# Kernel optimization log

Hardware: AMD Instinct MI355X
Metric: run time of the kernel (lower is better)

## Reference

```python
import jax, jax.numpy as jnp
import numpy as np

N = 50000
E = 800000
IN_CH = 256
ADIM = 64
EDIM = 16
NUM_CLUSTERS = 8


def setup_inputs() -> dict:
    key = jax.random.key(0)
    ks = jax.random.split(key, 16)
    def lin(k, fan_in, fan_out):
        w = jax.random.normal(k, (fan_in, fan_out), jnp.float32) * (fan_in ** -0.5)
        b = jnp.zeros((fan_out,), jnp.float32)
        return w, b
    W_down, b_down = lin(ks[0], IN_CH, ADIM)
    W_up, b_up = lin(ks[1], ADIM, IN_CH)
    W_time, b_time = lin(ks[2], EDIM, ADIM)
    Wq, bq = lin(ks[3], ADIM, ADIM)
    Wk, bk = lin(ks[4], ADIM, ADIM)
    Wv, bv = lin(ks[5], ADIM, ADIM)
    W_out, b_out = lin(ks[6], ADIM, ADIM)
    cluster_emb = jax.random.normal(ks[7], (NUM_CLUSTERS, ADIM), jnp.float32)
    x = jax.random.normal(ks[8], (N, IN_CH), jnp.float32)
    edge_attr = jax.random.normal(ks[9], (E, EDIM), jnp.float32)
    edge_index = jax.random.randint(ks[10], (2, E), 0, N, jnp.int32)
    return {"x": x, "edge_attr": edge_attr, "edge_index": edge_index,
            "W_down": W_down, "b_down": b_down, "W_up": W_up, "b_up": b_up,
            "W_time": W_time, "b_time": b_time, "Wq": Wq, "bq": bq,
            "Wk": Wk, "bk": bk, "Wv": Wv, "bv": bv,
            "cluster_emb": cluster_emb, "W_out": W_out, "b_out": b_out}


def reference(x, edge_attr, edge_index, W_down, b_down, W_up, b_up,
              W_time, b_time, Wq, bq, Wk, bk, Wv, bv, cluster_emb, W_out, b_out):
    n_nodes = x.shape[0]
    scaling = ADIM ** -0.5

    node_feat = jax.nn.relu(x @ W_down + b_down)              # [N, D]
    time_feat = jax.nn.relu(edge_attr @ W_time + b_time)      # [E, D]

    q = node_feat @ Wq + bq                                   # [N, D]
    k = time_feat @ Wk + bk                                   # [E, D]
    v = time_feat @ Wv + bv                                   # [E, D]

    # cluster assignment: argmax of softmax(sim) == argmax of sim
    sims = (time_feat @ cluster_emb.T) * scaling              # [E, C]
    cluster = jnp.argmax(sims, axis=-1).astype(jnp.int32)     # [E]

    src = edge_index[0]                                       # [E]
    q_i = q[src]                                              # [E, D]
    attn = jnp.sum(q_i * k, axis=-1) * scaling                # [E]

    # per-(cluster, src) segments replicate the per-cluster loop exactly
    seg = cluster * n_nodes + src                             # [E]
    num_seg = NUM_CLUSTERS * n_nodes

    # scatter_softmax within each (cluster, src) group (numerically stable)
    m = jax.ops.segment_max(attn, seg, num_segments=num_seg)
    ex = jnp.exp(attn - m[seg])
    denom = jax.ops.segment_sum(ex, seg, num_segments=num_seg)
    w = ex / denom[seg]                                       # [E]

    wv = v * w[:, None]                                       # [E, D]
    sums = jax.ops.segment_sum(wv, seg, num_segments=num_seg)
    sums = sums.reshape(NUM_CLUSTERS, n_nodes, ADIM)
    counts = jax.ops.segment_sum(jnp.ones((E,), jnp.float32), seg, num_segments=num_seg)
    counts = counts.reshape(NUM_CLUSTERS, n_nodes)
    mean = sums / jnp.maximum(counts, 1.0)[..., None]         # scatter_mean (0 where empty)

    # divide by number of non-empty clusters (len(outputs) in torch loop)
    edges_per_cluster = jax.ops.segment_sum(jnp.ones((E,), jnp.float32), cluster,
                                            num_segments=NUM_CLUSTERS)
    n_nonempty = jnp.sum((edges_per_cluster > 0).astype(jnp.float32))
    combined = jnp.sum(mean, axis=0) / n_nonempty             # [N, D]

    fused = jax.nn.relu(combined @ W_out + b_out)             # [N, D]
    out = x + (fused @ W_up + b_up)                           # [N, in_ch]
    return out
```

## Files before the change

kernel.cpp:

```cpp
#include <hip/hip_runtime.h>

#define NN 50000
#define EE 800000
#define INCH 256
#define D 64
#define ED 16
#define NC 8
#define NB 196
#define NEGINF (-3.0e38f)

__device__ __align__(16) char g_ws[64u << 20];

typedef __attribute__((ext_vector_type(8))) short bf16x8;
typedef __attribute__((ext_vector_type(4))) float f32x4;

__device__ __forceinline__ unsigned short f2b(float f){
  unsigned u = __float_as_uint(f);
  return (unsigned short)((u + 0x7fffu + ((u >> 16) & 1u)) >> 16);
}
__device__ __forceinline__ unsigned packbf(float lo, float hi){
  return (unsigned)f2b(lo) | ((unsigned)f2b(hi) << 16);
}
__device__ __forceinline__ float blo(unsigned w){ return __uint_as_float(w << 16); }
__device__ __forceinline__ float bhi(unsigned w){ return __uint_as_float(w & 0xffff0000u); }

union FragU { unsigned u[4]; uint4 q; bf16x8 b; };
__device__ __forceinline__ bf16x8 as_frag(unsigned a, unsigned b, unsigned c, unsigned d){
  FragU t; t.u[0]=a; t.u[1]=b; t.u[2]=c; t.u[3]=d; return t.b;
}
__device__ __forceinline__ bf16x8 ld_frag(const unsigned* p){
  FragU t; t.q = *(const uint4*)p; return t.b;
}
__device__ __forceinline__ void split2(float a, float b, unsigned &hi, unsigned &lo){
  hi = packbf(a, b);
  lo = packbf(a - blo(hi), b - bhi(hi));
}
__device__ __forceinline__ void mk_frags(float4 e0, float4 e1, bf16x8 &Ah, bf16x8 &Al){
  unsigned h0,h1,h2,h3,l0,l1,l2,l3;
  split2(e0.x, e0.y, h0, l0);
  split2(e0.z, e0.w, h1, l1);
  split2(e1.x, e1.y, h2, l2);
  split2(e1.z, e1.w, h3, l3);
  Ah = as_frag(h0,h1,h2,h3);
  Al = as_frag(l0,l1,l2,l3);
}

__global__ __launch_bounds__(256) void Adapter_30872224923942_kernel(
    unsigned* __restrict__ ws, int nwords)
{
  int stride = gridDim.x * 256;
  for (int i = blockIdx.x * 256 + threadIdx.x; i < nwords; i += stride)
    ws[i] = 0u;
}

__global__ __launch_bounds__(256) void kpre(
    const float* __restrict__ Wq, const float* __restrict__ bq,
    const float* __restrict__ Wk, const float* __restrict__ bk,
    const float* __restrict__ Wv, const float* __restrict__ bv,
    const float* __restrict__ Wo, const float* __restrict__ Wd,
    const float* __restrict__ Wu,
    float* __restrict__ cvec, float* __restrict__ u,
    float* __restrict__ s0, float* __restrict__ Wvo, float* __restrict__ bvo,
    unsigned* __restrict__ WdTP, unsigned* __restrict__ WuP,
    unsigned* __restrict__ MThP, unsigned* __restrict__ MTlP)
{
  int b = blockIdx.x, t = threadIdx.x;
  if (b < 16){
    int i = b*4 + (t >> 6), j = t & 63;
    float acc = 0.0f;
    for (int d = 0; d < D; ++d) acc = fmaf(Wv[i*D+d], Wo[d*D+j], acc);
    Wvo[i*D+j] = acc;
  } else if (b < 20){
    for (int k = 0; k < 8; ++k){
      int idx = (b-16)*2048 + t*8 + k;
      int col = idx >> 7, kw = idx & 127;
      WdTP[idx] = packbf(Wd[(2*kw)*D + col], Wd[(2*kw+1)*D + col]);
    }
  } else if (b < 24){
    for (int k = 0; k < 8; ++k){
      int idx = (b-20)*2048 + t*8 + k;
      int d2 = idx >> 8, c = idx & 255;
      WuP[idx] = packbf(Wu[(2*d2)*INCH + c], Wu[(2*d2+1)*INCH + c]);
    }
  } else if (b < 26){
    for (int k = 0; k < 4; ++k){
      int idx = (b-24)*1024 + t*4 + k;
      int j = idx >> 5, kw = idx & 31;
      float m0 = 0.0f, m1 = 0.0f;
      for (int d = 0; d < D; ++d) m0 = fmaf(Wq[(2*kw  )*D+d], Wk[j*D+d], m0);
      for (int d = 0; d < D; ++d) m1 = fmaf(Wq[(2*kw+1)*D+d], Wk[j*D+d], m1);
      unsigned hi = packbf(m0, m1);
      MThP[idx] = hi;
      MTlP[idx] = packbf(m0 - blo(hi), m1 - bhi(hi));
    }
  } else {
    if (t < 64){
      float acc = 0.0f;
      for (int d = 0; d < D; ++d) acc = fmaf(Wk[t*D+d], bq[d], acc);
      cvec[t] = acc;
    } else if (t < 128){
      int i = t - 64; float acc = 0.0f;
      for (int d = 0; d < D; ++d) acc = fmaf(Wq[i*D+d], bk[d], acc);
      u[i] = acc;
    } else if (t < 192){
      int j = t - 128; float acc = 0.0f;
      for (int d = 0; d < D; ++d) acc = fmaf(bv[d], Wo[d*D+j], acc);
      bvo[j] = acc;
    } else if (t == 192){
      float acc = 0.0f;
      for (int d = 0; d < D; ++d) acc = fmaf(bq[d], bk[d], acc);
      s0[0] = acc;
    }
  }
}

__global__ __launch_bounds__(256) void p1_hist(
    const int* __restrict__ eidx, int* __restrict__ cnt)
{
  int e = blockIdx.x * 256 + threadIdx.x;
  if (e < EE) atomicAdd(&cnt[eidx[e]], 1);
}

__global__ __launch_bounds__(256) void s1_scan(
    const int* __restrict__ cnt, int* __restrict__ rowptr, int* __restrict__ bsum)
{
  __shared__ int s[256];
  int t = threadIdx.x;
  int i = blockIdx.x * 256 + t;
  int v = (i < NN) ? cnt[i] : 0;
  s[t] = v; __syncthreads();
  #pragma unroll
  for (int off = 1; off < 256; off <<= 1){
    int add = (t >= off) ? s[t - off] : 0;
    __syncthreads();
    s[t] += add;
    __syncthreads();
  }
  if (i < NN) rowptr[i] = s[t] - v;
  if (t == 255) bsum[blockIdx.x] = s[255];
}
__global__ __launch_bounds__(256) void s2_scan(int* __restrict__ bsum)
{
  __shared__ int s[256];
  int t = threadIdx.x;
  int v = (t < NB) ? bsum[t] : 0;
  s[t] = v; __syncthreads();
  #pragma unroll
  for (int off = 1; off < 256; off <<= 1){
    int add = (t >= off) ? s[t - off] : 0;
    __syncthreads();
    s[t] += add;
    __syncthreads();
  }
  if (t < NB) bsum[t] = s[t] - v;
}
__global__ __launch_bounds__(256) void s3_add(
    int* __restrict__ rowptr, const int* __restrict__ bsum)
{
  int i = blockIdx.x * 256 + threadIdx.x;
  if (i < NN) rowptr[i] += bsum[blockIdx.x];
  if (i == 0) rowptr[NN] = EE;
}

__global__ __launch_bounds__(256) void p2_build(
    const int* __restrict__ eidx, const int* __restrict__ rowptr,
    int* __restrict__ fill, int2* __restrict__ pairS)
{
  int e = blockIdx.x * 256 + threadIdx.x;
  if (e >= EE) return;
  int src = eidx[e];
  int r = atomicAdd(&fill[src], 1);
  int2 pr; pr.x = e; pr.y = src;
  pairS[rowptr[src] + r] = pr;
}

__global__ __launch_bounds__(256) void k1_node(
    const float* __restrict__ x, const unsigned* __restrict__ WdTP,
    const float* __restrict__ bd,
    const unsigned* __restrict__ MThP, const unsigned* __restrict__ MTlP,
    const float* __restrict__ cvec, const float* __restrict__ u,
    const float* __restrict__ s0p,
    unsigned short* __restrict__ qkH, float* __restrict__ qb)
{
  __shared__ unsigned sWdT[8192];
  __shared__ unsigned sMTh[2048];
  __shared__ unsigned sMTl[2048];
  __shared__ float sNf[4][16][68];
  int t = threadIdx.x;
  int lane = t & 63;
  int w = t >> 6;
  int colA = lane & 15;
  int g = lane >> 4;
  int row0 = blockIdx.x * 64 + w * 16;

  int arow = row0 + colA;
  const float* xp = x + (size_t)min(arow, NN-1) * INCH + (g << 3);
  float4 xv[16];
  #pragma unroll
  for (int s = 0; s < 8; ++s){
    xv[2*s  ] = ((const float4*)(xp + s*32))[0];
    xv[2*s+1] = ((const float4*)(xp + s*32))[1];
  }
  #pragma unroll
  for (int i = 0; i < 8; ++i){
    int idx = 4*(t + 256*i);
    int col = idx >> 7;
    int dst = (idx & ~127) | ((idx & 127) ^ ((col & 7) << 2));
    *(uint4*)&sWdT[dst] = ((const uint4*)WdTP)[t + 256*i];
  }
  #pragma unroll
  for (int i = 0; i < 2; ++i){
    int idx = 4*(t + 256*i);
    int col = idx >> 5;
    int dst = (idx & ~31) | ((idx & 31) ^ ((col & 7) << 2));
    *(uint4*)&sMTh[dst] = ((const uint4*)MThP)[t + 256*i];
    *(uint4*)&sMTl[dst] = ((const uint4*)MTlP)[t + 256*i];
  }
  __syncthreads();

  f32x4 acc[4];
  #pragma unroll
  for (int nt = 0; nt < 4; ++nt){
    float bdc = bd[nt*16 + colA];
    acc[nt] = (f32x4){bdc, bdc, bdc, bdc};
  }
  #pragma unroll
  for (int s = 0; s < 8; ++s){
    bf16x8 Ah, Al;
    mk_frags(xv[2*s], xv[2*s+1], Ah, Al);
    #pragma unroll
    for (int nt = 0; nt < 4; ++nt){
      int col = nt*16 + colA;
      int kw = s*16 + g*4;
      bf16x8 B = ld_frag(&sWdT[col*128 + (kw ^ ((col & 7) << 2))]);
      acc[nt] = __builtin_amdgcn_mfma_f32_16x16x32_bf16(Ah, B, acc[nt], 0, 0, 0);
      acc[nt] = __builtin_amdgcn_mfma_f32_16x16x32_bf16(Al, B, acc[nt], 0, 0, 0);
    }
  }
  #pragma unroll
  for (int nt = 0; nt < 4; ++nt){
    #pragma unroll
    for (int q = 0; q < 4; ++q)
      sNf[w][g*4 + q][nt*16 + colA] = fmaxf(acc[nt][q], 0.0f);
  }

  {
    const float* nr = &sNf[w][colA][g*16];
    float b = 0.0f;
    #pragma unroll
    for (int c = 0; c < 16; ++c) b = fmaf(nr[c], u[g*16 + c], b);
    b += __shfl_xor(b, 16);
    b += __shfl_xor(b, 32);
    int qrow = row0 + colA;
    if (lane < 16 && qrow < NN) qb[qrow] = b + s0p[0];
  }

  f32x4 acc2[4];
  #pragma unroll
  for (int nt = 0; nt < 4; ++nt){
    float cvl = cvec[nt*16 + colA];
    acc2[nt] = (f32x4){cvl, cvl, cvl, cvl};
  }
  #pragma unroll
  for (int s = 0; s < 2; ++s){
    const float* ar = &sNf[w][colA][s*32 + g*8];
    float4 e0 = *(const float4*)(ar);
    float4 e1 = *(const float4*)(ar + 4);
    bf16x8 Ah, Al;
    mk_frags(e0, e1, Ah, Al);
    #pragma unroll
    for (int nt = 0; nt < 4; ++nt){
      int col = nt*16 + colA;
      int kw = s*16 + g*4;
      bf16x8 Bh = ld_frag(&sMTh[col*32 + (kw ^ ((col & 7) << 2))]);
      bf16x8 Bl = ld_frag(&sMTl[col*32 + (kw ^ ((col & 7) << 2))]);
      acc2[nt] = __builtin_amdgcn_mfma_f32_16x16x32_bf16(Ah, Bh, acc2[nt], 0, 0, 0);
      acc2[nt] = __builtin_amdgcn_mfma_f32_16x16x32_bf16(Al, Bh, acc2[nt], 0, 0, 0);
      acc2[nt] = __builtin_amdgcn_mfma_f32_16x16x32_bf16(Ah, Bl, acc2[nt], 0, 0, 0);
    }
  }
  #pragma unroll
  for (int nt = 0; nt < 4; ++nt){
    #pragma unroll
    for (int q = 0; q < 4; ++q){
      int r = row0 + g*4 + q;
      if (r < NN) qkH[(size_t)r * D + nt*16 + colA] = f2b(acc2[nt][q]);
    }
  }
}

__global__ __launch_bounds__(256) void p3_edge(
    const float* __restrict__ ea, const int* __restrict__ eidx,
    const float* __restrict__ Wt, const float* __restrict__ bt, const float* __restrict__ ce,
    const unsigned short* __restrict__ qkH, const float* __restrict__ qb,
    float* __restrict__ attnE, unsigned char* __restrict__ clE,
    unsigned* __restrict__ epc)
{
  __shared__ unsigned s_epc[NC];
  int t = threadIdx.x;
  if (t < NC) s_epc[t] = 0u;
  __syncthreads();
  int e0 = blockIdx.x * 512 + t;
  int e1 = e0 + 256;
  bool v1 = (e1 < EE);
  int e1c = v1 ? e1 : e0;
  int sA = eidx[e0];
  int sB = eidx[e1c];
  const float4* pa = (const float4*)(ea + (size_t)e0 * ED);
  float4 A0 = pa[0], A1 = pa[1], A2 = pa[2], A3 = pa[3];
  float qb0 = qb[sA];
  const float4* pb = (const float4*)(ea + (size_t)e1c * ED);
  float4 B0 = pb[0], B1 = pb[1], B2 = pb[2], B3 = pb[3];
  float qb1 = qb[sB];
  uint4 QA[8], QB[8];
  {
    const uint4* qp = (const uint4*)(qkH + (size_t)sA * D);
    #pragma unroll
    for (int i = 0; i < 8; ++i) QA[i] = qp[i];
  }
  {
    const uint4* qp = (const uint4*)(qkH + (size_t)sB * D);
    #pragma unroll
    for (int i = 0; i < 8; ++i) QB[i] = qp[i];
  }
  const float4* Wt4 = (const float4*)Wt;
  const float4* bt4 = (const float4*)bt;
  const float4* ce4 = (const float4*)ce;

  {
    float eav[ED] = {A0.x,A0.y,A0.z,A0.w, A1.x,A1.y,A1.z,A1.w,
                     A2.x,A2.y,A2.z,A2.w, A3.x,A3.y,A3.z,A3.w};
    float sims[NC];
    #pragma unroll
    for (int c = 0; c < NC; ++c) sims[c] = 0.0f;
    float at = qb0;
    #pragma unroll
    for (int d4 = 0; d4 < D/4; ++d4){
      float4 acc = bt4[d4];
      #pragma unroll
      for (int j = 0; j < ED; ++j){
        float4 wv = Wt4[j*(D/4) + d4];
        acc.x = fmaf(eav[j], wv.x, acc.x);
        acc.y = fmaf(eav[j], wv.y, acc.y);
        acc.z = fmaf(eav[j], wv.z, acc.z);
        acc.w = fmaf(eav[j], wv.w, acc.w);
      }
      float t0 = fmaxf(acc.x, 0.0f), t1 = fmaxf(acc.y, 0.0f);
      float t2 = fmaxf(acc.z, 0.0f), t3 = fmaxf(acc.w, 0.0f);
      #pragma unroll
      for (int c = 0; c < NC; ++c){
        float4 cv = ce4[c*(D/4) + d4];
        sims[c] = fmaf(t0, cv.x, sims[c]);
        sims[c] = fmaf(t1, cv.y, sims[c]);
        sims[c] = fmaf(t2, cv.z, sims[c]);
        sims[c] = fmaf(t3, cv.w, sims[c]);
      }
      uint4 qv = QA[d4 >> 1];
      unsigned w0 = (d4 & 1) ? qv.z : qv.x;
      unsigned w1 = (d4 & 1) ? qv.w : qv.y;
      at = fmaf(blo(w0), t0, at);
      at = fmaf(bhi(w0), t1, at);
      at = fmaf(blo(w1), t2, at);
      at = fmaf(bhi(w1), t3, at);
    }
    float best = NEGINF; int bc = 0;
    #pragma unroll
    for (int c = 0; c < NC; ++c){
      if (sims[c] > best){ best = sims[c]; bc = c; }
    }
    at *= 0.125f;
    attnE[e0] = at;
    clE[e0] = (unsigned char)bc;
    atomicAdd(&s_epc[bc], 1u);
  }

  if (v1){
    float eav[ED] = {B0.x,B0.y,B0.z,B0.w, B1.x,B1.y,B1.z,B1.w,
                     B2.x,B2.y,B2.z,B2.w, B3.x,B3.y,B3.z,B3.w};
    float sims[NC];
    #pragma unroll
    for (int c = 0; c < NC; ++c) sims[c] = 0.0f;
    float at = qb1;
    #pragma unroll
    for (int d4 = 0; d4 < D/4; ++d4){
      float4 acc = bt4[d4];
      #pragma unroll
      for (int j = 0; j < ED; ++j){
        float4 wv = Wt4[j*(D/4) + d4];
        acc.x = fmaf(eav[j], wv.x, acc.x);
        acc.y = fmaf(eav[j], wv.y, acc.y);
        acc.z = fmaf(eav[j], wv.z, acc.z);
        acc.w = fmaf(eav[j], wv.w, acc.w);
      }
      float t0 = fmaxf(acc.x, 0.0f), t1 = fmaxf(acc.y, 0.0f);
      float t2 = fmaxf(acc.z, 0.0f), t3 = fmaxf(acc.w, 0.0f);
      #pragma unroll
      for (int c = 0; c < NC; ++c){
        float4 cv = ce4[c*(D/4) + d4];
        sims[c] = fmaf(t0, cv.x, sims[c]);
        sims[c] = fmaf(t1, cv.y, sims[c]);
        sims[c] = fmaf(t2, cv.z, sims[c]);
        sims[c] = fmaf(t3, cv.w, sims[c]);
      }
      uint4 qv = QB[d4 >> 1];
      unsigned w0 = (d4 & 1) ? qv.z : qv.x;
      unsigned w1 = (d4 & 1) ? qv.w : qv.y;
      at = fmaf(blo(w0), t0, at);
      at = fmaf(bhi(w0), t1, at);
      at = fmaf(blo(w1), t2, at);
      at = fmaf(bhi(w1), t3, at);
    }
    float best = NEGINF; int bc = 0;
    #pragma unroll
    for (int c = 0; c < NC; ++c){
      if (sims[c] > best){ best = sims[c]; bc = c; }
    }
    at *= 0.125f;
    attnE[e1] = at;
    clE[e1] = (unsigned char)bc;
    atomicAdd(&s_epc[bc], 1u);
  }

  __syncthreads();
  if (t < NC){
    unsigned v = s_epc[t];
    if (v) atomicAdd(&epc[t], v);
  }
}

#define EROW 20
__global__ __launch_bounds__(256) void p4_node(
    const float* __restrict__ ea, const int2* __restrict__ pairS,
    const float* __restrict__ Wt, const float* __restrict__ bt,
    const float* __restrict__ attnE, const unsigned char* __restrict__ clE,
    const int* __restrict__ rowptr,
    float* __restrict__ T, float* __restrict__ S)
{
  __shared__ float s_den[4][NC];
  __shared__ int   s_cnt[4][NC];
  __shared__ float s_inv[4][NC];
  __shared__ float s_coef[4][64];
  __shared__ float s_ea[4][64][EROW];
  int t = threadIdx.x, lane = t & 63, w = t >> 6;
  float wl[ED];
  #pragma unroll
  for (int j = 0; j < ED; ++j) wl[j] = Wt[j*D + lane];
  float btl = bt[lane];
  if (lane < NC){ s_den[w][lane] = 0.0f; s_cnt[w][lane] = 0; }
  int node = blockIdx.x * 4 + w;
  int start = rowptr[node], end = rowptr[node + 1];
  for (int base = start; base < end; base += 64){
    int idx = base + lane;
    if (idx < end){
      int e = pairS[idx].x;
      float ex = __expf(attnE[e]);
      int c = clE[e];
      atomicAdd(&s_den[w][c], ex);
      atomicAdd(&s_cnt[w][c], 1);
    }
  }
  if (lane < NC){
    int   cc = s_cnt[w][lane];
    float dd = s_den[w][lane];
    s_inv[w][lane] = (cc > 0) ? 1.0f / (dd * (float)cc) : 0.0f;
    float sv = (cc > 0) ? 1.0f / (float)cc : 0.0f;
    sv += __shfl_xor(sv, 1); sv += __shfl_xor(sv, 2); sv += __shfl_xor(sv, 4);
    if (lane == 0) S[node] = sv;
  }
  float Tacc = 0.0f;
  for (int base = start; base < end; base += 64){
    int idx = base + lane;
    if (idx < end){
      int e = pairS[idx].x;
      s_coef[w][lane] = __expf(attnE[e]) * s_inv[w][clE[e]];
    }
    #pragma unroll
    for (int r = 0; r < 4; ++r){
      int slot = base + r*16 + (lane >> 2);
      if (slot < end){
        int e = pairS[slot].x;
        float4 v = ((const float4*)ea)[(size_t)e*4 + (lane & 3)];
        *(float4*)&s_ea[w][slot - base][(lane & 3)*4] = v;
      }
    }
    int mm = min(64, end - base);
    for (int tt = 0; tt < mm; ++tt){
      float coef = s_coef[w][tt];
      const float4* er = (const float4*)&s_ea[w][tt][0];
      float4 e0 = er[0], e1 = er[1], e2 = er[2], e3 = er[3];
      float tfv = btl;
      tfv = fmaf(e0.x, wl[0], tfv);  tfv = fmaf(e0.y, wl[1], tfv);
      tfv = fmaf(e0.z, wl[2], tfv);  tfv = fmaf(e0.w, wl[3], tfv);
      tfv = fmaf(e1.x, wl[4], tfv);  tfv = fmaf(e1.y, wl[5], tfv);
      tfv = fmaf(e1.z, wl[6], tfv);  tfv = fmaf(e1.w, wl[7], tfv);
      tfv = fmaf(e2.x, wl[8], tfv);  tfv = fmaf(e2.y, wl[9], tfv);
      tfv = fmaf(e2.z, wl[10], tfv); tfv = fmaf(e2.w, wl[11], tfv);
      tfv = fmaf(e3.x, wl[12], tfv); tfv = fmaf(e3.y, wl[13], tfv);
      tfv = fmaf(e3.z, wl[14], tfv); tfv = fmaf(e3.w, wl[15], tfv);
      tfv = fmaxf(tfv, 0.0f);
      Tacc = fmaf(coef, tfv, Tacc);
    }
  }
  T[(size_t)node * D + lane] = Tacc;
}

__global__ __launch_bounds__(256) void k5_out(
    const float* __restrict__ x, const float* __restrict__ T, const float* __restrict__ S,
    const float* __restrict__ Wvo, const float* __restrict__ bvo,
    const unsigned* __restrict__ WuP, const float* __restrict__ bu,
    const float* __restrict__ bo, const unsigned* __restrict__ epc,
    float* __restrict__ out)
{
  __shared__ unsigned sWuP[8192];
  __shared__ float s_fu[16*64];
  int t = threadIdx.x;
  #pragma unroll
  for (int i = 0; i < 8; ++i)
    ((uint4*)sWuP)[t + 256*i] = ((const uint4*)WuP)[t + 256*i];
  int lane = t & 63;
  int wg = __builtin_amdgcn_readfirstlane(t >> 6);
  int n0 = blockIdx.x * 16 + wg * 4;
  float nne = 0.0f;
  #pragma unroll
  for (int c = 0; c < NC; ++c) nne += (epc[c] > 0u) ? 1.0f : 0.0f;
  float inv = 1.0f / fmaxf(nne, 1.0f);
  float T0 = T[(size_t)(n0+0)*D + lane];
  float T1 = T[(size_t)(n0+1)*D + lane];
  float T2 = T[(size_t)(n0+2)*D + lane];
  float T3 = T[(size_t)(n0+3)*D + lane];
  float bvl = bvo[lane], bol = bo[lane];
  float f0 = S[n0+0]*bvl, f1 = S[n0+1]*bvl, f2 = S[n0+2]*bvl, f3 = S[n0+3]*bvl;
  #pragma unroll 8
  for (int i = 0; i < 64; ++i){
    float wv = Wvo[i*64 + lane];
    f0 = fmaf(__shfl(T0, i), wv, f0);
    f1 = fmaf(__shfl(T1, i), wv, f1);
    f2 = fmaf(__shfl(T2, i), wv, f2);
    f3 = fmaf(__shfl(T3, i), wv, f3);
  }
  f0 = fmaxf(f0*inv + bol, 0.0f);
  f1 = fmaxf(f1*inv + bol, 0.0f);
  f2 = fmaxf(f2*inv + bol, 0.0f);
  f3 = fmaxf(f3*inv + bol, 0.0f);
  s_fu[(wg*4+0)*64 + lane] = f0;
  s_fu[(wg*4+1)*64 + lane] = f1;
  s_fu[(wg*4+2)*64 + lane] = f2;
  s_fu[(wg*4+3)*64 + lane] = f3;
  __syncthreads();
  float4 bu4 = ((const float4*)bu)[lane];
  float4 o0 = ((const float4*)(x + (size_t)(n0+0)*INCH))[lane];
  float4 o1 = ((const float4*)(x + (size_t)(n0+1)*INCH))[lane];
  float4 o2 = ((const float4*)(x + (size_t)(n0+2)*INCH))[lane];
  float4 o3 = ((const float4*)(x + (size_t)(n0+3)*INCH))[lane];
  o0.x += bu4.x; o0.y += bu4.y; o0.z += bu4.z; o0.w += bu4.w;
  o1.x += bu4.x; o1.y += bu4.y; o1.z += bu4.z; o1.w += bu4.w;
  o2.x += bu4.x; o2.y += bu4.y; o2.z += bu4.z; o2.w += bu4.w;
  o3.x += bu4.x; o3.y += bu4.y; o3.z += bu4.z; o3.w += bu4.w;
  const float2* fu2 = (const float2*)s_fu;
  #pragma unroll 4
  for (int d2 = 0; d2 < 32; ++d2){
    uint4 wp = *(const uint4*)&sWuP[d2*256 + lane*4];
    float4 wlv = { blo(wp.x), blo(wp.y), blo(wp.z), blo(wp.w) };
    float4 wh  = { bhi(wp.x), bhi(wp.y), bhi(wp.z), bhi(wp.w) };
    float2 g0 = fu2[(wg*4+0)*32 + d2];
    float2 g1 = fu2[(wg*4+1)*32 + d2];
    float2 g2 = fu2[(wg*4+2)*32 + d2];
    float2 g3 = fu2[(wg*4+3)*32 + d2];
    o0.x = fmaf(g0.x, wlv.x, o0.x); o0.y = fmaf(g0.x, wlv.y, o0.y);
    o0.z = fmaf(g0.x, wlv.z, o0.z); o0.w = fmaf(g0.x, wlv.w, o0.w);
    o0.x = fmaf(g0.y, wh.x, o0.x);  o0.y = fmaf(g0.y, wh.y, o0.y);
    o0.z = fmaf(g0.y, wh.z, o0.z);  o0.w = fmaf(g0.y, wh.w, o0.w);
    o1.x = fmaf(g1.x, wlv.x, o1.x); o1.y = fmaf(g1.x, wlv.y, o1.y);
    o1.z = fmaf(g1.x, wlv.z, o1.z); o1.w = fmaf(g1.x, wlv.w, o1.w);
    o1.x = fmaf(g1.y, wh.x, o1.x);  o1.y = fmaf(g1.y, wh.y, o1.y);
    o1.z = fmaf(g1.y, wh.z, o1.z);  o1.w = fmaf(g1.y, wh.w, o1.w);
    o2.x = fmaf(g2.x, wlv.x, o2.x); o2.y = fmaf(g2.x, wlv.y, o2.y);
    o2.z = fmaf(g2.x, wlv.z, o2.z); o2.w = fmaf(g2.x, wlv.w, o2.w);
    o2.x = fmaf(g2.y, wh.x, o2.x);  o2.y = fmaf(g2.y, wh.y, o2.y);
    o2.z = fmaf(g2.y, wh.z, o2.z);  o2.w = fmaf(g2.y, wh.w, o2.w);
    o3.x = fmaf(g3.x, wlv.x, o3.x); o3.y = fmaf(g3.x, wlv.y, o3.y);
    o3.z = fmaf(g3.x, wlv.z, o3.z); o3.w = fmaf(g3.x, wlv.w, o3.w);
    o3.x = fmaf(g3.y, wh.x, o3.x);  o3.y = fmaf(g3.y, wh.y, o3.y);
    o3.z = fmaf(g3.y, wh.z, o3.z);  o3.w = fmaf(g3.y, wh.w, o3.w);
  }
  ((float4*)(out + (size_t)(n0+0)*INCH))[lane] = o0;
  ((float4*)(out + (size_t)(n0+1)*INCH))[lane] = o1;
  ((float4*)(out + (size_t)(n0+2)*INCH))[lane] = o2;
  ((float4*)(out + (size_t)(n0+3)*INCH))[lane] = o3;
}

extern "C" void kernel_launch(void* const* d_in, const int* in_sizes, int n_in,
                              void* d_out, int out_size, void* d_ws, size_t ws_size,
                              hipStream_t stream)
{
  const float* x  = (const float*)d_in[0];
  const float* ea = (const float*)d_in[1];
  const int* eidx = (const int*)d_in[2];
  const float* Wd = (const float*)d_in[3];  const float* bd = (const float*)d_in[4];
  const float* Wu = (const float*)d_in[5];  const float* bu = (const float*)d_in[6];
  const float* Wt = (const float*)d_in[7];  const float* bt = (const float*)d_in[8];
  const float* Wq = (const float*)d_in[9];  const float* bq = (const float*)d_in[10];
  const float* Wk = (const float*)d_in[11]; const float* bk = (const float*)d_in[12];
  const float* Wv = (const float*)d_in[13]; const float* bv = (const float*)d_in[14];
  const float* ce = (const float*)d_in[15];
  const float* Wo = (const float*)d_in[16]; const float* bo = (const float*)d_in[17];
  float* out = (float*)d_out;

  size_t need = 0;
  need += (size_t)NN*4;
  need += (size_t)NN*4;
  need += 64;
  size_t zbytes = need;
  need += (size_t)(NN+4)*4;
  need += 1024;
  need += (size_t)NN*D*2;
  need += (size_t)NN*4;
  need += (size_t)EE*8;
  need += (size_t)EE*4;
  need += (size_t)EE;
  need += 16;
  need += (size_t)NN*D*4;
  need += (size_t)NN*4;
  need += 256 + 256 + 16 + 4096*4 + 256;
  need += 8192*4 + 8192*4;
  need += 2048*4 + 2048*4;

  char* w = (char*)d_ws;
  if (ws_size < need){
    void* p = nullptr;
    hipGetSymbolAddress(&p, HIP_SYMBOL(g_ws));
    w = (char*)p;
  }
  size_t off = 0;
  int*      cnt    = (int*)(w + off);      off += (size_t)NN*4;
  int*      fill   = (int*)(w + off);      off += (size_t)NN*4;
  unsigned* epc    = (unsigned*)(w + off); off += 64;
  int*      rowptr = (int*)(w + off);      off += (size_t)(NN+4)*4;
  int*      bsum   = (int*)(w + off);      off += 1024;
  unsigned short* qkH = (unsigned short*)(w + off); off += (size_t)NN*D*2;
  float*    qb     = (float*)(w + off);    off += (size_t)NN*4;
  int2*     pairS  = (int2*)(w + off);     off += (size_t)EE*8;
  float*    attnE  = (float*)(w + off);    off += (size_t)EE*4;
  unsigned char* clE = (unsigned char*)(w + off); off += (size_t)EE;
  off = (off + 15) & ~(size_t)15;
  float*    T      = (float*)(w + off);    off += (size_t)NN*D*4;
  float*    S      = (float*)(w + off);    off += (size_t)NN*4;
  float*    cvec   = (float*)(w + off);    off += 256;
  float*    u      = (float*)(w + off);    off += 256;
  float*    s0     = (float*)(w + off);    off += 16;
  float*    Wvo    = (float*)(w + off);    off += 4096*4;
  float*    bvo    = (float*)(w + off);    off += 256;
  unsigned* WdTP   = (unsigned*)(w + off); off += 8192*4;
  unsigned* WuP    = (unsigned*)(w + off); off += 8192*4;
  unsigned* MThP   = (unsigned*)(w + off); off += 2048*4;
  unsigned* MTlP   = (unsigned*)(w + off); off += 2048*4;

  int zwords = (int)(zbytes / 4);
  Adapter_30872224923942_kernel<<<dim3(128), dim3(256), 0, stream>>>((unsigned*)w, zwords);
  kpre<<<dim3(27), dim3(256), 0, stream>>>(Wq, bq, Wk, bk, Wv, bv, Wo, Wd, Wu,
                                           cvec, u, s0, Wvo, bvo, WdTP, WuP, MThP, MTlP);
  p1_hist<<<dim3(EE/256), dim3(256), 0, stream>>>(eidx, cnt);
  s1_scan<<<dim3(NB), dim3(256), 0, stream>>>(cnt, rowptr, bsum);
  s2_scan<<<dim3(1),  dim3(256), 0, stream>>>(bsum);
  s3_add <<<dim3(NB), dim3(256), 0, stream>>>(rowptr, bsum);
  p2_build<<<dim3(EE/256), dim3(256), 0, stream>>>(eidx, rowptr, fill, pairS);
  k1_node<<<dim3((NN + 63)/64), dim3(256), 0, stream>>>(x, WdTP, bd, MThP, MTlP,
                                                        cvec, u, s0, qkH, qb);
  p3_edge<<<dim3((EE + 511)/512), dim3(256), 0, stream>>>(ea, eidx, Wt, bt, ce, qkH, qb,
                                                          attnE, clE, epc);
  p4_node<<<dim3(NN/4), dim3(256), 0, stream>>>(ea, pairS, Wt, bt, attnE, clE, rowptr, T, S);
  k5_out <<<dim3(NN/16), dim3(256), 0, stream>>>(x, T, S, Wvo, bvo, WuP, bu, bo, epc, out);
}
```

Baseline: 432.1 us.

## Compute per-edge time features in p4_node with split-bf16 MFMA

Replaces the scalar FMA loop that recomputes relu(edge_attr @ W_time + b) for each edge in p4_node with 16x16x32 bf16 MFMA tiles. Both edge attributes and W_time are split into hi/lo bf16 parts and combined with three MFMAs to keep near-fp32 accuracy. W_time is pre-packed in kpre, and a cross-lane shuffle reduction produces the per-node output. This removes per-lane scalar FLOPs on the gather-heavy node pass, but adds bf16 conversion and LDS write overhead, and only 16 of the 32 K slots do useful work.

Result: slower. 459.4 us (+6.3%).

```diff
diff --git a/kernel.cpp b/kernel.cpp
--- a/kernel.cpp
+++ b/kernel.cpp
@@ -58,11 +58,12 @@
     const float* __restrict__ Wk, const float* __restrict__ bk,
     const float* __restrict__ Wv, const float* __restrict__ bv,
     const float* __restrict__ Wo, const float* __restrict__ Wd,
-    const float* __restrict__ Wu,
+    const float* __restrict__ Wu, const float* __restrict__ Wt,
     float* __restrict__ cvec, float* __restrict__ u,
     float* __restrict__ s0, float* __restrict__ Wvo, float* __restrict__ bvo,
     unsigned* __restrict__ WdTP, unsigned* __restrict__ WuP,
-    unsigned* __restrict__ MThP, unsigned* __restrict__ MTlP)
+    unsigned* __restrict__ MThP, unsigned* __restrict__ MTlP,
+    unsigned* __restrict__ WtTPh, unsigned* __restrict__ WtTPl)
 {
   int b = blockIdx.x, t = threadIdx.x;
   if (b < 16){
@@ -92,6 +93,15 @@
       unsigned hi = packbf(m0, m1);
       MThP[idx] = hi;
       MTlP[idx] = packbf(m0 - blo(hi), m1 - bhi(hi));
+    }
+  } else if (b < 27){
+    for (int k = 0; k < 4; ++k){
+      int idx = t*4 + k;
+      int col = idx >> 4, kw = idx & 15;
+      unsigned hi = 0u, lo = 0u;
+      if (kw < 8) split2(Wt[(2*kw)*D + col], Wt[(2*kw+1)*D + col], hi, lo);
+      WtTPh[idx] = hi;
+      WtTPl[idx] = lo;
     }
   } else {
     if (t < 64){
@@ -428,10 +438,10 @@
   }
 }
 
-#define EROW 20
 __global__ __launch_bounds__(256) void p4_node(
     const float* __restrict__ ea, const int2* __restrict__ pairS,
-    const float* __restrict__ Wt, const float* __restrict__ bt,
+    const unsigned* __restrict__ WtTPh, const unsigned* __restrict__ WtTPl,
+    const float* __restrict__ bt,
     const float* __restrict__ attnE, const unsigned char* __restrict__ clE,
     const int* __restrict__ rowptr,
     float* __restrict__ T, float* __restrict__ S)
@@ -440,12 +450,28 @@
   __shared__ int   s_cnt[4][NC];
   __shared__ float s_inv[4][NC];
   __shared__ float s_coef[4][64];
-  __shared__ float s_ea[4][64][EROW];
+  __shared__ unsigned s_eah[4][64][16];
+  __shared__ unsigned s_eal[4][64][16];
   int t = threadIdx.x, lane = t & 63, w = t >> 6;
-  float wl[ED];
-  #pragma unroll
-  for (int j = 0; j < ED; ++j) wl[j] = Wt[j*D + lane];
-  float btl = bt[lane];
+  int colA = lane & 15, g = lane >> 4;
+  bf16x8 Bh[4], Bl[4];
+  #pragma unroll
+  for (int nt = 0; nt < 4; ++nt){
+    int col = nt*16 + colA;
+    Bh[nt] = ld_frag(&WtTPh[col*16 + g*4]);
+    Bl[nt] = ld_frag(&WtTPl[col*16 + g*4]);
+  }
+  float btc[4];
+  #pragma unroll
+  for (int nt = 0; nt < 4; ++nt) btc[nt] = bt[nt*16 + colA];
+  {
+    uint4 z = {0u,0u,0u,0u};
+    #pragma unroll
+    for (int i = 0; i < 4; ++i){
+      *(uint4*)&s_eah[w][lane][i*4] = z;
+      *(uint4*)&s_eal[w][lane][i*4] = z;
+    }
+  }
   if (lane < NC){ s_den[w][lane] = 0.0f; s_cnt[w][lane] = 0; }
   int node = blockIdx.x * 4 + w;
   int start = rowptr[node], end = rowptr[node + 1];
@@ -467,41 +493,56 @@
     sv += __shfl_xor(sv, 1); sv += __shfl_xor(sv, 2); sv += __shfl_xor(sv, 4);
     if (lane == 0) S[node] = sv;
   }
-  float Tacc = 0.0f;
+  float Tacc[4] = {0.0f, 0.0f, 0.0f, 0.0f};
   for (int base = start; base < end; base += 64){
     int idx = base + lane;
+    float cf = 0.0f;
     if (idx < end){
       int e = pairS[idx].x;
-      s_coef[w][lane] = __expf(attnE[e]) * s_inv[w][clE[e]];
-    }
+      cf = __expf(attnE[e]) * s_inv[w][clE[e]];
+    }
+    s_coef[w][lane] = cf;
     #pragma unroll
     for (int r = 0; r < 4; ++r){
       int slot = base + r*16 + (lane >> 2);
       if (slot < end){
         int e = pairS[slot].x;
         float4 v = ((const float4*)ea)[(size_t)e*4 + (lane & 3)];
-        *(float4*)&s_ea[w][slot - base][(lane & 3)*4] = v;
+        unsigned h0,l0,h1,l1;
+        split2(v.x, v.y, h0, l0);
+        split2(v.z, v.w, h1, l1);
+        int row = slot - base, kw = (lane & 3)*2;
+        s_eah[w][row][kw] = h0; s_eah[w][row][kw+1] = h1;
+        s_eal[w][row][kw] = l0; s_eal[w][row][kw+1] = l1;
       }
     }
     int mm = min(64, end - base);
-    for (int tt = 0; tt < mm; ++tt){
-      float coef = s_coef[w][tt];
-      const float4* er = (const float4*)&s_ea[w][tt][0];
-      float4 e0 = er[0], e1 = er[1], e2 = er[2], e3 = er[3];
-      float tfv = btl;
-      tfv = fmaf(e0.x, wl[0], tfv);  tfv = fmaf(e0.y, wl[1], tfv);
-      tfv = fmaf(e0.z, wl[2], tfv);  tfv = fmaf(e0.w, wl[3], tfv);
-      tfv = fmaf(e1.x, wl[4], tfv);  tfv = fmaf(e1.y, wl[5], tfv);
-      tfv = fmaf(e1.z, wl[6], tfv);  tfv = fmaf(e1.w, wl[7], tfv);
-      tfv = fmaf(e2.x, wl[8], tfv);  tfv = fmaf(e2.y, wl[9], tfv);
-      tfv = fmaf(e2.z, wl[10], tfv); tfv = fmaf(e2.w, wl[11], tfv);
-      tfv = fmaf(e3.x, wl[12], tfv); tfv = fmaf(e3.y, wl[13], tfv);
-      tfv = fmaf(e3.z, wl[14], tfv); tfv = fmaf(e3.w, wl[15], tfv);
-      tfv = fmaxf(tfv, 0.0f);
-      Tacc = fmaf(coef, tfv, Tacc);
-    }
-  }
-  T[(size_t)node * D + lane] = Tacc;
+    for (int tile = 0; tile*16 < mm; ++tile){
+      bf16x8 Ah = ld_frag(&s_eah[w][tile*16 + colA][g*4]);
+      bf16x8 Al = ld_frag(&s_eal[w][tile*16 + colA][g*4]);
+      float4 cf4 = *(const float4*)&s_coef[w][tile*16 + g*4];
+      #pragma unroll
+      for (int nt = 0; nt < 4; ++nt){
+        f32x4 acc = (f32x4){btc[nt], btc[nt], btc[nt], btc[nt]};
+        acc = __builtin_amdgcn_mfma_f32_16x16x32_bf16(Ah, Bh[nt], acc, 0, 0, 0);
+        acc = __builtin_amdgcn_mfma_f32_16x16x32_bf16(Al, Bh[nt], acc, 0, 0, 0);
+        acc = __builtin_amdgcn_mfma_f32_16x16x32_bf16(Ah, Bl[nt], acc, 0, 0, 0);
+        float f0 = fmaxf(acc[0], 0.0f), f1 = fmaxf(acc[1], 0.0f);
+        float f2 = fmaxf(acc[2], 0.0f), f3 = fmaxf(acc[3], 0.0f);
+        Tacc[nt] = fmaf(cf4.x, f0, Tacc[nt]);
+        Tacc[nt] = fmaf(cf4.y, f1, Tacc[nt]);
+        Tacc[nt] = fmaf(cf4.z, f2, Tacc[nt]);
+        Tacc[nt] = fmaf(cf4.w, f3, Tacc[nt]);
+      }
+    }
+  }
+  #pragma unroll
+  for (int nt = 0; nt < 4; ++nt){
+    float v = Tacc[nt];
+    v += __shfl_xor(v, 16);
+    v += __shfl_xor(v, 32);
+    if (g == 0) T[(size_t)node * D + nt*16 + colA] = v;
+  }
 }
 
 __global__ __launch_bounds__(256) void k5_out(
@@ -624,6 +665,7 @@
   need += 256 + 256 + 16 + 4096*4 + 256;
   need += 8192*4 + 8192*4;
   need += 2048*4 + 2048*4;
+  need += 1024*4 + 1024*4;
 
   char* w = (char*)d_ws;
   if (ws_size < need){
@@ -654,11 +696,14 @@
   unsigned* WuP    = (unsigned*)(w + off); off += 8192*4;
   unsigned* MThP   = (unsigned*)(w + off); off += 2048*4;
   unsigned* MTlP   = (unsigned*)(w + off); off += 2048*4;
+  unsigned* WtTPh  = (unsigned*)(w + off); off += 1024*4;
+  unsigned* WtTPl  = (unsigned*)(w + off); off += 1024*4;
 
   int zwords = (int)(zbytes / 4);
   Adapter_30872224923942_kernel<<<dim3(128), dim3(256), 0, stream>>>((unsigned*)w, zwords);
-  kpre<<<dim3(27), dim3(256), 0, stream>>>(Wq, bq, Wk, bk, Wv, bv, Wo, Wd, Wu,
-                                           cvec, u, s0, Wvo, bvo, WdTP, WuP, MThP, MTlP);
+  kpre<<<dim3(28), dim3(256), 0, stream>>>(Wq, bq, Wk, bk, Wv, bv, Wo, Wd, Wu, Wt,
+                                           cvec, u, s0, Wvo, bvo, WdTP, WuP,
+                                           MThP, MTlP, WtTPh, WtTPl);
   p1_hist<<<dim3(EE/256), dim3(256), 0, stream>>>(eidx, cnt);
   s1_scan<<<dim3(NB), dim3(256), 0, stream>>>(cnt, rowptr, bsum);
   s2_scan<<<dim3(1),  dim3(256), 0, stream>>>(bsum);
@@ -668,6 +713,7 @@
                                                         cvec, u, s0, qkH, qb);
   p3_edge<<<dim3((EE + 511)/512), dim3(256), 0, stream>>>(ea, eidx, Wt, bt, ce, qkH, qb,
                                                           attnE, clE, epc);
-  p4_node<<<dim3(NN/4), dim3(256), 0, stream>>>(ea, pairS, Wt, bt, attnE, clE, rowptr, T, S);
+  p4_node<<<dim3(NN/4), dim3(256), 0, stream>>>(ea, pairS, WtTPh, WtTPl, bt,
+                                                attnE, clE, rowptr, T, S);
   k5_out <<<dim3(NN/16), dim3(256), 0, stream>>>(x, T, S, Wvo, bvo, WuP, bu, bo, epc, out);
 }
```

## Fuse softmax denominator and count accumulation into edge kernel via global atomics

Applied to the files above, without the earlier changes.

The edge kernel now adds exp(attn) and a count into per-(cluster, source) global arrays with atomics. This removes the separate histogram kernel and the first pass over each node's edges in the node kernel. Node counts for the CSR scan are rebuilt by summing the per-cluster counts, and the scan and build kernels are moved after the edge kernel. The cost is 1.6M global float and int atomics, plus two extra zeroed 1.6MB arrays. The kernel also adds unused packed Wt bf16 tables in kpre, which is dead work.

Measured after the change: 444.6 us. +2.9%, slower.

```diff
diff --git a/kernel.cpp b/kernel.cpp
--- a/kernel.cpp
+++ b/kernel.cpp
@@ -58,11 +58,12 @@
     const float* __restrict__ Wk, const float* __restrict__ bk,
     const float* __restrict__ Wv, const float* __restrict__ bv,
     const float* __restrict__ Wo, const float* __restrict__ Wd,
-    const float* __restrict__ Wu,
+    const float* __restrict__ Wu, const float* __restrict__ Wt,
     float* __restrict__ cvec, float* __restrict__ u,
     float* __restrict__ s0, float* __restrict__ Wvo, float* __restrict__ bvo,
     unsigned* __restrict__ WdTP, unsigned* __restrict__ WuP,
-    unsigned* __restrict__ MThP, unsigned* __restrict__ MTlP)
+    unsigned* __restrict__ MThP, unsigned* __restrict__ MTlP,
+    unsigned* __restrict__ WtTPh, unsigned* __restrict__ WtTPl)
 {
   int b = blockIdx.x, t = threadIdx.x;
   if (b < 16){
@@ -92,6 +93,15 @@
       unsigned hi = packbf(m0, m1);
       MThP[idx] = hi;
       MTlP[idx] = packbf(m0 - blo(hi), m1 - bhi(hi));
+    }
+  } else if (b < 27){
+    for (int k = 0; k < 4; ++k){
+      int idx = t*4 + k;
+      int col = idx >> 4, kw = idx & 15;
+      unsigned hi = 0u, lo = 0u;
+      if (kw < 8) split2(Wt[(2*kw)*D + col], Wt[(2*kw+1)*D + col], hi, lo);
+      WtTPh[idx] = hi;
+      WtTPl[idx] = lo;
     }
   } else {
     if (t < 64){
@@ -114,11 +124,16 @@
   }
 }
 
-__global__ __launch_bounds__(256) void p1_hist(
-    const int* __restrict__ eidx, int* __restrict__ cnt)
-{
-  int e = blockIdx.x * 256 + threadIdx.x;
-  if (e < EE) atomicAdd(&cnt[eidx[e]], 1);
+__global__ __launch_bounds__(256) void pc_cnt(
+    const int* __restrict__ cntG, int* __restrict__ cnt)
+{
+  int i = blockIdx.x * 256 + threadIdx.x;
+  if (i < NN){
+    int s = 0;
+    #pragma unroll
+    for (int c = 0; c < NC; ++c) s += cntG[c*NN + i];
+    cnt[i] = s;
+  }
 }
 
 __global__ __launch_bounds__(256) void s1_scan(
@@ -294,7 +309,8 @@
     const float* __restrict__ Wt, const float* __restrict__ bt, const float* __restrict__ ce,
     const unsigned short* __restrict__ qkH, const float* __restrict__ qb,
     float* __restrict__ attnE, unsigned char* __restrict__ clE,
-    unsigned* __restrict__ epc)
+    unsigned* __restrict__ epc,
+    float* __restrict__ denG, int* __restrict__ cntG)
 {
   __shared__ unsigned s_epc[NC];
   int t = threadIdx.x;
@@ -372,6 +388,9 @@
     attnE[e0] = at;
     clE[e0] = (unsigned char)bc;
     atomicAdd(&s_epc[bc], 1u);
+    float ex = __expf(at);
+    atomicAdd(&denG[bc*NN + sA], ex);
+    atomicAdd(&cntG[bc*NN + sA], 1);
   }
 
   if (v1){
@@ -419,6 +438,9 @@
     attnE[e1] = at;
     clE[e1] = (unsigned char)bc;
     atomicAdd(&s_epc[bc], 1u);
+    float ex = __expf(at);
+    atomicAdd(&denG[bc*NN + sB], ex);
+    atomicAdd(&cntG[bc*NN + sB], 1);
   }
 
   __syncthreads();
@@ -434,10 +456,9 @@
     const float* __restrict__ Wt, const float* __restrict__ bt,
     const float* __restrict__ attnE, const unsigned char* __restrict__ clE,
     const int* __restrict__ rowptr,
+    const float* __restrict__ denG, const int* __restrict__ cntG,
     float* __restrict__ T, float* __restrict__ S)
 {
-  __shared__ float s_den[4][NC];
-  __shared__ int   s_cnt[4][NC];
   __shared__ float s_inv[4][NC];
   __shared__ float s_coef[4][64];
   __shared__ float s_ea[4][64][EROW];
@@ -446,27 +467,16 @@
   #pragma unroll
   for (int j = 0; j < ED; ++j) wl[j] = Wt[j*D + lane];
   float btl = bt[lane];
-  if (lane < NC){ s_den[w][lane] = 0.0f; s_cnt[w][lane] = 0; }
   int node = blockIdx.x * 4 + w;
-  int start = rowptr[node], end = rowptr[node + 1];
-  for (int base = start; base < end; base += 64){
-    int idx = base + lane;
-    if (idx < end){
-      int e = pairS[idx].x;
-      float ex = __expf(attnE[e]);
-      int c = clE[e];
-      atomicAdd(&s_den[w][c], ex);
-      atomicAdd(&s_cnt[w][c], 1);
-    }
-  }
   if (lane < NC){
-    int   cc = s_cnt[w][lane];
-    float dd = s_den[w][lane];
+    float dd = denG[lane*NN + node];
+    int   cc = cntG[lane*NN + node];
     s_inv[w][lane] = (cc > 0) ? 1.0f / (dd * (float)cc) : 0.0f;
     float sv = (cc > 0) ? 1.0f / (float)cc : 0.0f;
     sv += __shfl_xor(sv, 1); sv += __shfl_xor(sv, 2); sv += __shfl_xor(sv, 4);
     if (lane == 0) S[node] = sv;
   }
+  int start = rowptr[node], end = rowptr[node + 1];
   float Tacc = 0.0f;
   for (int base = start; base < end; base += 64){
     int idx = base + lane;
@@ -610,6 +620,8 @@
   need += (size_t)NN*4;
   need += (size_t)NN*4;
   need += 64;
+  need += (size_t)NN*NC*4;
+  need += (size_t)NN*NC*4;
   size_t zbytes = need;
   need += (size_t)(NN+4)*4;
   need += 1024;
@@ -624,6 +636,7 @@
   need += 256 + 256 + 16 + 4096*4 + 256;
   need += 8192*4 + 8192*4;
   need += 2048*4 + 2048*4;
+  need += 1024*4 + 1024*4;
 
   char* w = (char*)d_ws;
   if (ws_size < need){
@@ -635,6 +648,8 @@
   int*      cnt    = (int*)(w + off);      off += (size_t)NN*4;
   int*      fill   = (int*)(w + off);      off += (size_t)NN*4;
   unsigned* epc    = (unsigned*)(w + off); off += 64;
+  float*    denG   = (float*)(w + off);    off += (size_t)NN*NC*4;
+  int*      cntG   = (int*)(w + off);      off += (size_t)NN*NC*4;
   int*      rowptr = (int*)(w + off);      off += (size_t)(NN+4)*4;
   int*      bsum   = (int*)(w + off);      off += 1024;
   unsigned short* qkH = (unsigned short*)(w + off); off += (size_t)NN*D*2;
@@ -654,20 +669,24 @@
   unsigned* WuP    = (unsigned*)(w + off); off += 8192*4;
   unsigned* MThP   = (unsigned*)(w + off); off += 2048*4;
   unsigned* MTlP   = (unsigned*)(w + off); off += 2048*4;
+  unsigned* WtTPh  = (unsigned*)(w + off); off += 1024*4;
+  unsigned* WtTPl  = (unsigned*)(w + off); off += 1024*4;
 
   int zwords = (int)(zbytes / 4);
   Adapter_30872224923942_kernel<<<dim3(128), dim3(256), 0, stream>>>((unsigned*)w, zwords);
-  kpre<<<dim3(27), dim3(256), 0, stream>>>(Wq, bq, Wk, bk, Wv, bv, Wo, Wd, Wu,
-                                           cvec, u, s0, Wvo, bvo, WdTP, WuP, MThP, MTlP);
-  p1_hist<<<dim3(EE/256), dim3(256), 0, stream>>>(eidx, cnt);
+  kpre<<<dim3(28), dim3(256), 0, stream>>>(Wq, bq, Wk, bk, Wv, bv, Wo, Wd, Wu, Wt,
+                                           cvec, u, s0, Wvo, bvo, WdTP, WuP,
+                                           MThP, MTlP, WtTPh, WtTPl);
+  k1_node<<<dim3((NN + 63)/64), dim3(256), 0, stream>>>(x, WdTP, bd, MThP, MTlP,
+                                                        cvec, u, s0, qkH, qb);
+  p3_edge<<<dim3((EE + 511)/512), dim3(256), 0, stream>>>(ea, eidx, Wt, bt, ce, qkH, qb,
+                                                          attnE, clE, epc, denG, cntG);
+  pc_cnt<<<dim3(NB), dim3(256), 0, stream>>>(cntG, cnt);
   s1_scan<<<dim3(NB), dim3(256), 0, stream>>>(cnt, rowptr, bsum);
   s2_scan<<<dim3(1),  dim3(256), 0, stream>>>(bsum);
   s3_add <<<dim3(NB), dim3(256), 0, stream>>>(rowptr, bsum);
   p2_build<<<dim3(EE/256), dim3(256), 0, stream>>>(eidx, rowptr, fill, pairS);
-  k1_node<<<dim3((NN + 63)/64), dim3(256), 0, stream>>>(x, WdTP, bd, MThP, MTlP,
-                                                        cvec, u, s0, qkH, qb);
-  p3_edge<<<dim3((EE + 511)/512), dim3(256), 0, stream>>>(ea, eidx, Wt, bt, ce, qkH, qb,
-                                                          attnE, clE, epc);
-  p4_node<<<dim3(NN/4), dim3(256), 0, stream>>>(ea, pairS, Wt, bt, attnE, clE, rowptr, T, S);
+  p4_node<<<dim3(NN/4), dim3(256), 0, stream>>>(ea, pairS, Wt, bt, attnE, clE, rowptr,
+                                                denG, cntG, T, S);
   k5_out <<<dim3(NN/16), dim3(256), 0, stream>>>(x, T, S, Wvo, bvo, WuP, bu, bo, epc, out);
 }
```
